# Performance work log

Measured on AMD Instinct MI355X. Metric: run time of the kernel, lower is better.

Reference implementation:

```python
import jax, jax.numpy as jnp
import numpy as np

B, S, H = 4, 2048, 1024

def setup_inputs() -> dict:
    key = jax.random.key(0)
    k = jax.random.split(key, 5)
    scale = 1.0 / np.sqrt(H)
    return {
        "hidden": jax.random.normal(k[0], (B, S, H), dtype=jnp.float32),
        "mask": jnp.zeros((B, 1, S, S), dtype=jnp.float32),
        "R": jax.random.normal(k[1], (S, S), dtype=jnp.float32),
        "G_w": jax.random.normal(k[2], (H, H), dtype=jnp.float32) * scale,
        "G_b": jnp.zeros((H,), dtype=jnp.float32),
        "F_w": jax.random.normal(k[3], (H, H), dtype=jnp.float32) * scale,
        "F_b": jnp.zeros((H,), dtype=jnp.float32),
    }

def reference(hidden, mask, R, G_w, G_b, F_w, F_b):
    # scores: [B, S, S] = learned random bias + additive attention mask
    scores = R + mask[:, 0]
    probs = jax.nn.softmax(scores, axis=-1)  # dropout is identity in eval mode
    values = jnp.einsum('bsh,oh->bso', hidden, G_w) + G_b  # G_linear
    out = jnp.einsum('bqk,bkh->bqh', probs, values)
    out = jnp.einsum('bsh,oh->bso', out, F_w) + F_b  # final_linear
    return out
```

## Files before the change

### kernel.cpp

```cpp
#include <hip/hip_runtime.h>
#include <hip/hip_bf16.h>

typedef __bf16 bf16x8 __attribute__((ext_vector_type(8)));
typedef __bf16 bf16x4 __attribute__((ext_vector_type(4)));
typedef float  f32x4  __attribute__((ext_vector_type(4)));
typedef float  f32x16 __attribute__((ext_vector_type(16)));

#define GPTR(p) ((__attribute__((address_space(1))) void*)(p))
#define LPTR(p) ((__attribute__((address_space(3))) void*)(p))

__global__ __launch_bounds__(256) void cvt_kernel(const float* __restrict__ x,
                                                  __bf16* __restrict__ y, long n) {
    long i = ((long)blockIdx.x * 256 + threadIdx.x) * 8;
    if (i >= n) return;
    float4 a = *reinterpret_cast<const float4*>(x + i);
    float4 c = *reinterpret_cast<const float4*>(x + i + 4);
    bf16x8 o;
    o[0] = (__bf16)a.x; o[1] = (__bf16)a.y; o[2] = (__bf16)a.z; o[3] = (__bf16)a.w;
    o[4] = (__bf16)c.x; o[5] = (__bf16)c.y; o[6] = (__bf16)c.z; o[7] = (__bf16)c.w;
    *reinterpret_cast<bf16x8*>(y + i) = o;
}

__global__ __launch_bounds__(256) void transpose_cvt_kernel(const float* __restrict__ x,
                                                            __bf16* __restrict__ y, int n) {
    __shared__ float tile[64][65];
    const int bx = blockIdx.x * 64;
    const int by = blockIdx.y * 64;
    const int t = threadIdx.x;
    const int tr = t >> 4;
    const int tc = (t & 15) * 4;
#pragma unroll
    for (int i = 0; i < 4; i++) {
        float4 v = *reinterpret_cast<const float4*>(&x[(size_t)(by + tr + i * 16) * n + bx + tc]);
        tile[tr + i * 16][tc + 0] = v.x;
        tile[tr + i * 16][tc + 1] = v.y;
        tile[tr + i * 16][tc + 2] = v.z;
        tile[tr + i * 16][tc + 3] = v.w;
    }
    __syncthreads();
    const int wr = t >> 2;
    const int wc = (t & 3) * 16;
    bf16x8 o0, o1;
#pragma unroll
    for (int j = 0; j < 8; j++) o0[j] = (__bf16)tile[wc + j][wr];
#pragma unroll
    for (int j = 0; j < 8; j++) o1[j] = (__bf16)tile[wc + 8 + j][wr];
    *reinterpret_cast<bf16x8*>(&y[(size_t)(bx + wr) * n + by + wc]) = o0;
    *reinterpret_cast<bf16x8*>(&y[(size_t)(bx + wr) * n + by + wc + 8]) = o1;
}

__global__ __launch_bounds__(256) void gemv_bias_kernel(const float* __restrict__ Fw,
                                                        const float* __restrict__ Gb,
                                                        const float* __restrict__ Fb,
                                                        float* __restrict__ b2, int H) {
    const int o = blockIdx.x;
    float s = 0.f;
    for (int h = threadIdx.x; h < H; h += 256) s += Fw[(size_t)o * H + h] * Gb[h];
#pragma unroll
    for (int off = 32; off > 0; off >>= 1) s += __shfl_xor(s, off);
    __shared__ float ss[4];
    if ((threadIdx.x & 63) == 0) ss[threadIdx.x >> 6] = s;
    __syncthreads();
    if (threadIdx.x == 0) b2[o] = ss[0] + ss[1] + ss[2] + ss[3] + Fb[o];
}

__global__ __launch_bounds__(256) void softmax_kernel(const float* __restrict__ R,
                                                      const float* __restrict__ mask,
                                                      __bf16* __restrict__ P, int S) {
    const int q = blockIdx.x, b = blockIdx.y;
    const int t = threadIdx.x;
    const int lane = t & 63, wave = t >> 6;
    const float* rrow = R + (size_t)q * S;
    const float* mrow = mask + ((size_t)b * S + q) * (size_t)S;
    __bf16* prow = P + ((size_t)b * S + q) * (size_t)S;

    float v[8];
#pragma unroll
    for (int i = 0; i < 2; i++) {
        float4 r4 = *reinterpret_cast<const float4*>(rrow + t * 8 + i * 4);
        float4 m4 = *reinterpret_cast<const float4*>(mrow + t * 8 + i * 4);
        v[i * 4 + 0] = r4.x + m4.x;
        v[i * 4 + 1] = r4.y + m4.y;
        v[i * 4 + 2] = r4.z + m4.z;
        v[i * 4 + 3] = r4.w + m4.w;
    }
    float mx = v[0];
#pragma unroll
    for (int i = 1; i < 8; i++) mx = fmaxf(mx, v[i]);
#pragma unroll
    for (int off = 32; off > 0; off >>= 1) mx = fmaxf(mx, __shfl_xor(mx, off));
    __shared__ float smax[4], ssum[4];
    if (lane == 0) smax[wave] = mx;
    __syncthreads();
    mx = fmaxf(fmaxf(smax[0], smax[1]), fmaxf(smax[2], smax[3]));
    float sum = 0.f;
#pragma unroll
    for (int i = 0; i < 8; i++) { v[i] = __expf(v[i] - mx); sum += v[i]; }
#pragma unroll
    for (int off = 32; off > 0; off >>= 1) sum += __shfl_xor(sum, off);
    if (lane == 0) ssum[wave] = sum;
    __syncthreads();
    sum = ssum[0] + ssum[1] + ssum[2] + ssum[3];
    const float inv = 1.0f / sum;
    bf16x8 o;
#pragma unroll
    for (int i = 0; i < 8; i++) o[i] = (__bf16)(v[i] * inv);
    *reinterpret_cast<bf16x8*>(prow + t * 8) = o;
}

template <bool TRANSC, bool CFLOAT, bool BIAS>
__global__ __launch_bounds__(256) void gemm_nt_kernel(
    const __bf16* __restrict__ A, const __bf16* __restrict__ B,
    const float* __restrict__ bias, void* __restrict__ Cv,
    int K, int lda, int ldb, int ldc,
    long strideA, long strideB, long strideC) {
    const int t = threadIdx.x;
    const int lane = t & 63;
    const int wave = t >> 6;
    const int lane31 = lane & 31;
    const int hi = lane >> 5;
    const int wm = (wave >> 1) * 64;
    const int wn = (wave & 1) * 64;
    const int bm = blockIdx.y * 128;
    const int bn = blockIdx.x * 128;
    const int bz = blockIdx.z;

    A += (size_t)bz * strideA;
    B += (size_t)bz * strideB;

    __shared__ __bf16 As[128 * 64];
    __shared__ __bf16 Bs[128 * 64];

    const int rsub = lane >> 3;
    const int csub = lane & 7;
    const int lchunk = csub ^ rsub;
    const __bf16* ga0 = A + (size_t)(bm + wave * 32 + rsub) * lda + lchunk * 8;
    const __bf16* gb0 = B + (size_t)(bn + wave * 32 + rsub) * ldb + lchunk * 8;

    f32x16 acc[2][2];
#pragma unroll
    for (int i = 0; i < 2; i++)
#pragma unroll
        for (int j = 0; j < 2; j++) acc[i][j] = (f32x16)(0.f);

    for (int kt = 0; kt < K; kt += 64) {
        __syncthreads();
#pragma unroll
        for (int c = 0; c < 4; c++)
            __builtin_amdgcn_global_load_lds(GPTR(ga0 + (size_t)(c * 8) * lda + kt),
                                             LPTR(&As[(wave * 32 + c * 8) * 64]), 16, 0, 0);
#pragma unroll
        for (int c = 0; c < 4; c++)
            __builtin_amdgcn_global_load_lds(GPTR(gb0 + (size_t)(c * 8) * ldb + kt),
                                             LPTR(&Bs[(wave * 32 + c * 8) * 64]), 16, 0, 0);
        __syncthreads();
#pragma unroll
        for (int s = 0; s < 4; s++) {
            bf16x8 af[2], bfr[2];
#pragma unroll
            for (int mi = 0; mi < 2; mi++) {
                const int r = wm + mi * 32 + lane31;
                af[mi] = *reinterpret_cast<const bf16x8*>(
                    &As[r * 64 + (((2 * s + hi) ^ (r & 7)) << 3)]);
            }
#pragma unroll
            for (int ni = 0; ni < 2; ni++) {
                const int r = wn + ni * 32 + lane31;
                bfr[ni] = *reinterpret_cast<const bf16x8*>(
                    &Bs[r * 64 + (((2 * s + hi) ^ (r & 7)) << 3)]);
            }
#pragma unroll
            for (int mi = 0; mi < 2; mi++)
#pragma unroll
                for (int ni = 0; ni < 2; ni++)
                    acc[mi][ni] = __builtin_amdgcn_mfma_f32_32x32x16_bf16(af[mi], bfr[ni], acc[mi][ni], 0, 0, 0);
        }
    }

    __bf16* Cb = (__bf16*)Cv + (size_t)bz * strideC;
    float* Cf = (float*)Cv + (size_t)bz * strideC;
#pragma unroll
    for (int mi = 0; mi < 2; mi++) {
#pragma unroll
        for (int ni = 0; ni < 2; ni++) {
            const int cm = bm + wm + mi * 32;
            const int cn = bn + wn + ni * 32 + lane31;
            const float bv = BIAS ? bias[cn] : 0.0f;
#pragma unroll
            for (int rq = 0; rq < 4; rq++) {
                const int rbase = rq * 8 + 4 * hi;
                if constexpr (TRANSC) {
                    bf16x4 pk;
#pragma unroll
                    for (int rr = 0; rr < 4; rr++) pk[rr] = (__bf16)(acc[mi][ni][rq * 4 + rr] + bv);
                    *reinterpret_cast<bf16x4*>(Cb + (size_t)cn * ldc + cm + rbase) = pk;
                } else if constexpr (CFLOAT) {
#pragma unroll
                    for (int rr = 0; rr < 4; rr++)
                        Cf[(size_t)(cm + rbase + rr) * ldc + cn] = acc[mi][ni][rq * 4 + rr] + bv;
                } else {
#pragma unroll
                    for (int rr = 0; rr < 4; rr++)
                        Cb[(size_t)(cm + rbase + rr) * ldc + cn] = (__bf16)(acc[mi][ni][rq * 4 + rr] + bv);
                }
            }
        }
    }
}

__global__ __launch_bounds__(256) void gemm_nt64_kernel(
    const __bf16* __restrict__ A, const __bf16* __restrict__ B,
    __bf16* __restrict__ C, int K, int lda, int ldb, int ldc) {
    const int t = threadIdx.x;
    const int lane = t & 63;
    const int wave = t >> 6;
    const int lane31 = lane & 31;
    const int hi = lane >> 5;
    const int wm = (wave >> 1) * 32;
    const int wn = (wave & 1) * 32;
    const int bm = blockIdx.y * 64;
    const int bn = blockIdx.x * 64;

    __shared__ __bf16 As[64 * 64];
    __shared__ __bf16 Bs[64 * 64];

    const int rsub = lane >> 3;
    const int csub = lane & 7;
    const int lchunk = csub ^ rsub;
    const __bf16* ga0 = A + (size_t)(bm + wave * 16 + rsub) * lda + lchunk * 8;
    const __bf16* gb0 = B + (size_t)(bn + wave * 16 + rsub) * ldb + lchunk * 8;

    f32x16 acc = (f32x16)(0.f);

    for (int kt = 0; kt < K; kt += 64) {
        __syncthreads();
#pragma unroll
        for (int c = 0; c < 2; c++)
            __builtin_amdgcn_global_load_lds(GPTR(ga0 + (size_t)(c * 8) * lda + kt),
                                             LPTR(&As[(wave * 16 + c * 8) * 64]), 16, 0, 0);
#pragma unroll
        for (int c = 0; c < 2; c++)
            __builtin_amdgcn_global_load_lds(GPTR(gb0 + (size_t)(c * 8) * ldb + kt),
                                             LPTR(&Bs[(wave * 16 + c * 8) * 64]), 16, 0, 0);
        __syncthreads();
#pragma unroll
        for (int s = 0; s < 4; s++) {
            const int ra = wm + lane31;
            const int rb = wn + lane31;
            bf16x8 af = *reinterpret_cast<const bf16x8*>(
                &As[ra * 64 + (((2 * s + hi) ^ (ra & 7)) << 3)]);
            bf16x8 bfr = *reinterpret_cast<const bf16x8*>(
                &Bs[rb * 64 + (((2 * s + hi) ^ (rb & 7)) << 3)]);
            acc = __builtin_amdgcn_mfma_f32_32x32x16_bf16(af, bfr, acc, 0, 0, 0);
        }
    }

    const int cm = bm + wm;
    const int cn = bn + wn + lane31;
#pragma unroll
    for (int rq = 0; rq < 4; rq++) {
        const int rbase = rq * 8 + 4 * hi;
#pragma unroll
        for (int rr = 0; rr < 4; rr++)
            C[(size_t)(cm + rbase + rr) * ldc + cn] = (__bf16)acc[rq * 4 + rr];
    }
}

extern "C" void kernel_launch(void* const* d_in, const int* in_sizes, int n_in,
                              void* d_out, int out_size, void* d_ws, size_t ws_size,
                              hipStream_t stream) {
    const float* hidden = (const float*)d_in[0];
    const float* mask   = (const float*)d_in[1];
    const float* R      = (const float*)d_in[2];
    const float* G_w    = (const float*)d_in[3];
    const float* G_b    = (const float*)d_in[4];
    const float* F_w    = (const float*)d_in[5];
    const float* F_b    = (const float*)d_in[6];
    float* out = (float*)d_out;

    constexpr int B = 4, S = 2048, H = 1024;
    char* ws = (char*)d_ws;
    __bf16* h_bf  = (__bf16*)(ws);
    __bf16* vt    = (__bf16*)(ws + (16ll << 20));
    __bf16* probs = (__bf16*)(ws + (32ll << 20));
    __bf16* Wm    = (__bf16*)(ws + (32ll << 20));
    __bf16* f_bf  = (__bf16*)(ws + (64ll << 20));
    __bf16* gt_bf = (__bf16*)(ws + (66ll << 20));
    float*  b2    = (float*)(ws + (64ll << 20));

    cvt_kernel<<<(H * H) / 8 / 256, 256, 0, stream>>>(F_w, f_bf, (long)H * H);
    transpose_cvt_kernel<<<dim3(H / 64, H / 64), 256, 0, stream>>>(G_w, gt_bf, H);

    gemm_nt64_kernel<<<dim3(H / 64, H / 64), 256, 0, stream>>>(
        f_bf, gt_bf, Wm, H, H, H, H);

    gemv_bias_kernel<<<H, 256, 0, stream>>>(F_w, G_b, F_b, b2, H);

    cvt_kernel<<<(B * S * H) / 8 / 256, 256, 0, stream>>>(hidden, h_bf, (long)B * S * H);

    gemm_nt_kernel<true, false, false><<<dim3(H / 128, S / 128, B), 256, 0, stream>>>(
        h_bf, Wm, nullptr, vt, H, H, H,  S,
        (long)S * H, 0, (long)H * S);

    softmax_kernel<<<dim3(S, B), 256, 0, stream>>>(R, mask, probs, S);

    gemm_nt_kernel<false, true, true><<<dim3(H / 128, S / 128, B), 256, 0, stream>>>(
        probs, vt, b2, out, S, S, S, H,
        (long)S * S, (long)H * S, (long)S * H);
}
```

Measured before the change: 257.1 us.

## Merge prep kernels into two phases, add XCD block swizzle and LDS-staged transposed store

Merges the conversion, transpose, bias GEMV, weight GEMM and softmax kernels into two multi-role launches. Blocks are dispatched by block index so independent work in each phase overlaps and fewer launches are needed. The final GEMM remaps its 1D block IDs so that blocks on the same XCD share a batch and row band, to improve L2 reuse. The transposed value GEMM now stages its output through LDS so that global writes are coalesced 16-byte stores instead of strided 8-byte ones. The cost is more divergent branching per launch and extra LDS traffic and barriers in the epilogue.

```diff
diff --git a/kernel.cpp b/kernel.cpp
--- a/kernel.cpp
+++ b/kernel.cpp
@@ -9,106 +9,171 @@
 #define GPTR(p) ((__attribute__((address_space(1))) void*)(p))
 #define LPTR(p) ((__attribute__((address_space(3))) void*)(p))
 
-__global__ __launch_bounds__(256) void cvt_kernel(const float* __restrict__ x,
-                                                  __bf16* __restrict__ y, long n) {
-    long i = ((long)blockIdx.x * 256 + threadIdx.x) * 8;
-    if (i >= n) return;
-    float4 a = *reinterpret_cast<const float4*>(x + i);
-    float4 c = *reinterpret_cast<const float4*>(x + i + 4);
-    bf16x8 o;
-    o[0] = (__bf16)a.x; o[1] = (__bf16)a.y; o[2] = (__bf16)a.z; o[3] = (__bf16)a.w;
-    o[4] = (__bf16)c.x; o[5] = (__bf16)c.y; o[6] = (__bf16)c.z; o[7] = (__bf16)c.w;
-    *reinterpret_cast<bf16x8*>(y + i) = o;
+__global__ __launch_bounds__(256) void phase_a_kernel(
+    const float* __restrict__ hidden, __bf16* __restrict__ h_bf,
+    const float* __restrict__ Fw, __bf16* __restrict__ f_bf,
+    const float* __restrict__ Gw, __bf16* __restrict__ gt_bf,
+    const float* __restrict__ Gb, const float* __restrict__ Fb,
+    float* __restrict__ b2, int H) {
+    __shared__ float tile[64][65];
+    const int blk = blockIdx.x;
+    const int t = threadIdx.x;
+
+    if (blk < 4096) {
+        long i = ((long)blk * 256 + t) * 8;
+        float4 a = *reinterpret_cast<const float4*>(hidden + i);
+        float4 c = *reinterpret_cast<const float4*>(hidden + i + 4);
+        bf16x8 o;
+        o[0] = (__bf16)a.x; o[1] = (__bf16)a.y; o[2] = (__bf16)a.z; o[3] = (__bf16)a.w;
+        o[4] = (__bf16)c.x; o[5] = (__bf16)c.y; o[6] = (__bf16)c.z; o[7] = (__bf16)c.w;
+        *reinterpret_cast<bf16x8*>(h_bf + i) = o;
+    } else if (blk < 4608) {
+        long i = ((long)(blk - 4096) * 256 + t) * 8;
+        float4 a = *reinterpret_cast<const float4*>(Fw + i);
+        float4 c = *reinterpret_cast<const float4*>(Fw + i + 4);
+        bf16x8 o;
+        o[0] = (__bf16)a.x; o[1] = (__bf16)a.y; o[2] = (__bf16)a.z; o[3] = (__bf16)a.w;
+        o[4] = (__bf16)c.x; o[5] = (__bf16)c.y; o[6] = (__bf16)c.z; o[7] = (__bf16)c.w;
+        *reinterpret_cast<bf16x8*>(f_bf + i) = o;
+    } else if (blk < 4864) {
+        const int id = blk - 4608;
+        const int bx = (id & 15) * 64;
+        const int by = (id >> 4) * 64;
+        const int tr = t >> 4;
+        const int tc = (t & 15) * 4;
+#pragma unroll
+        for (int i = 0; i < 4; i++) {
+            float4 v = *reinterpret_cast<const float4*>(&Gw[(size_t)(by + tr + i * 16) * H + bx + tc]);
+            tile[tr + i * 16][tc + 0] = v.x;
+            tile[tr + i * 16][tc + 1] = v.y;
+            tile[tr + i * 16][tc + 2] = v.z;
+            tile[tr + i * 16][tc + 3] = v.w;
+        }
+        __syncthreads();
+        const int wr = t >> 2;
+        const int wc = (t & 3) * 16;
+        bf16x8 o0, o1;
+#pragma unroll
+        for (int j = 0; j < 8; j++) o0[j] = (__bf16)tile[wc + j][wr];
+#pragma unroll
+        for (int j = 0; j < 8; j++) o1[j] = (__bf16)tile[wc + 8 + j][wr];
+        *reinterpret_cast<bf16x8*>(&gt_bf[(size_t)(bx + wr) * H + by + wc]) = o0;
+        *reinterpret_cast<bf16x8*>(&gt_bf[(size_t)(bx + wr) * H + by + wc + 8]) = o1;
+    } else {
+        const int o = blk - 4864;
+        float s = 0.f;
+        for (int h = t; h < H; h += 256) s += Fw[(size_t)o * H + h] * Gb[h];
+#pragma unroll
+        for (int off = 32; off > 0; off >>= 1) s += __shfl_xor(s, off);
+        __shared__ float ss[4];
+        if ((t & 63) == 0) ss[t >> 6] = s;
+        __syncthreads();
+        if (t == 0) b2[o] = ss[0] + ss[1] + ss[2] + ss[3] + Fb[o];
+    }
 }
 
-__global__ __launch_bounds__(256) void transpose_cvt_kernel(const float* __restrict__ x,
-                                                            __bf16* __restrict__ y, int n) {
-    __shared__ float tile[64][65];
-    const int bx = blockIdx.x * 64;
-    const int by = blockIdx.y * 64;
+__global__ __launch_bounds__(256) void phase_b_kernel(
+    const __bf16* __restrict__ f_bf, const __bf16* __restrict__ gt_bf,
+    __bf16* __restrict__ Wm, const float* __restrict__ R,
+    const float* __restrict__ mask, __bf16* __restrict__ P, int H, int S) {
+    const int blk = blockIdx.x;
     const int t = threadIdx.x;
-    const int tr = t >> 4;
-    const int tc = (t & 15) * 4;
-#pragma unroll
-    for (int i = 0; i < 4; i++) {
-        float4 v = *reinterpret_cast<const float4*>(&x[(size_t)(by + tr + i * 16) * n + bx + tc]);
-        tile[tr + i * 16][tc + 0] = v.x;
-        tile[tr + i * 16][tc + 1] = v.y;
-        tile[tr + i * 16][tc + 2] = v.z;
-        tile[tr + i * 16][tc + 3] = v.w;
-    }
-    __syncthreads();
-    const int wr = t >> 2;
-    const int wc = (t & 3) * 16;
-    bf16x8 o0, o1;
-#pragma unroll
-    for (int j = 0; j < 8; j++) o0[j] = (__bf16)tile[wc + j][wr];
-#pragma unroll
-    for (int j = 0; j < 8; j++) o1[j] = (__bf16)tile[wc + 8 + j][wr];
-    *reinterpret_cast<bf16x8*>(&y[(size_t)(bx + wr) * n + by + wc]) = o0;
-    *reinterpret_cast<bf16x8*>(&y[(size_t)(bx + wr) * n + by + wc + 8]) = o1;
+
+    if (blk < 256) {
+        __shared__ __bf16 As[64 * 64];
+        __shared__ __bf16 Bs[64 * 64];
+        const int lane = t & 63;
+        const int wave = t >> 6;
+        const int lane31 = lane & 31;
+        const int hi = lane >> 5;
+        const int wm = (wave >> 1) * 32;
+        const int wn = (wave & 1) * 32;
+        const int bm = (blk >> 4) * 64;
+        const int bn = (blk & 15) * 64;
+
+        const int rsub = lane >> 3;
+        const int csub = lane & 7;
+        const int lchunk = csub ^ rsub;
+        const __bf16* ga0 = f_bf + (size_t)(bm + wave * 16 + rsub) * H + lchunk * 8;
+        const __bf16* gb0 = gt_bf + (size_t)(bn + wave * 16 + rsub) * H + lchunk * 8;
+
+        f32x16 acc = (f32x16)(0.f);
+        for (int kt = 0; kt < H; kt += 64) {
+            __syncthreads();
+#pragma unroll
+            for (int c = 0; c < 2; c++)
+                __builtin_amdgcn_global_load_lds(GPTR(ga0 + (size_t)(c * 8) * H + kt),
+                                                 LPTR(&As[(wave * 16 + c * 8) * 64]), 16, 0, 0);
+#pragma unroll
+            for (int c = 0; c < 2; c++)
+                __builtin_amdgcn_global_load_lds(GPTR(gb0 + (size_t)(c * 8) * H + kt),
+                                                 LPTR(&Bs[(wave * 16 + c * 8) * 64]), 16, 0, 0);
+            __syncthreads();
+#pragma unroll
+            for (int s = 0; s < 4; s++) {
+                const int ra = wm + lane31;
+                const int rb = wn + lane31;
+                bf16x8 af = *reinterpret_cast<const bf16x8*>(
+                    &As[ra * 64 + (((2 * s + hi) ^ (ra & 7)) << 3)]);
+                bf16x8 bfr = *reinterpret_cast<const bf16x8*>(
+                    &Bs[rb * 64 + (((2 * s + hi) ^ (rb & 7)) << 3)]);
+                acc = __builtin_amdgcn_mfma_f32_32x32x16_bf16(af, bfr, acc, 0, 0, 0);
+            }
+        }
+        const int cm = bm + wm;
+        const int cn = bn + wn + lane31;
+#pragma unroll
+        for (int rq = 0; rq < 4; rq++) {
+            const int rbase = rq * 8 + 4 * hi;
+#pragma unroll
+            for (int rr = 0; rr < 4; rr++)
+                Wm[(size_t)(cm + rbase + rr) * H + cn] = (__bf16)acc[rq * 4 + rr];
+        }
+    } else {
+        const int id = blk - 256;
+        const int b = id >> 11;
+        const int q = id & 2047;
+        const int lane = t & 63, wave = t >> 6;
+        const float* rrow = R + (size_t)q * S;
+        const float* mrow = mask + ((size_t)b * S + q) * (size_t)S;
+        __bf16* prow = P + ((size_t)b * S + q) * (size_t)S;
+
+        float v[8];
+#pragma unroll
+        for (int i = 0; i < 2; i++) {
+            float4 r4 = *reinterpret_cast<const float4*>(rrow + t * 8 + i * 4);
+            float4 m4 = *reinterpret_cast<const float4*>(mrow + t * 8 + i * 4);
+            v[i * 4 + 0] = r4.x + m4.x;
+            v[i * 4 + 1] = r4.y + m4.y;
+            v[i * 4 + 2] = r4.z + m4.z;
+            v[i * 4 + 3] = r4.w + m4.w;
+        }
+        float mx = v[0];
+#pragma unroll
+        for (int i = 1; i < 8; i++) mx = fmaxf(mx, v[i]);
+#pragma unroll
+        for (int off = 32; off > 0; off >>= 1) mx = fmaxf(mx, __shfl_xor(mx, off));
+        __shared__ float smax[4], ssum[4];
+        if (lane == 0) smax[wave] = mx;
+        __syncthreads();
+        mx = fmaxf(fmaxf(smax[0], smax[1]), fmaxf(smax[2], smax[3]));
+        float sum = 0.f;
+#pragma unroll
+        for (int i = 0; i < 8; i++) { v[i] = __expf(v[i] - mx); sum += v[i]; }
+#pragma unroll
+        for (int off = 32; off > 0; off >>= 1) sum += __shfl_xor(sum, off);
+        if (lane == 0) ssum[wave] = sum;
+        __syncthreads();
+        sum = ssum[0] + ssum[1] + ssum[2] + ssum[3];
+        const float inv = 1.0f / sum;
+        bf16x8 o;
+#pragma unroll
+        for (int i = 0; i < 8; i++) o[i] = (__bf16)(v[i] * inv);
+        *reinterpret_cast<bf16x8*>(prow + t * 8) = o;
+    }
 }
 
-__global__ __launch_bounds__(256) void gemv_bias_kernel(const float* __restrict__ Fw,
-                                                        const float* __restrict__ Gb,
-                                                        const float* __restrict__ Fb,
-                                                        float* __restrict__ b2, int H) {
-    const int o = blockIdx.x;
-    float s = 0.f;
-    for (int h = threadIdx.x; h < H; h += 256) s += Fw[(size_t)o * H + h] * Gb[h];
-#pragma unroll
-    for (int off = 32; off > 0; off >>= 1) s += __shfl_xor(s, off);
-    __shared__ float ss[4];
-    if ((threadIdx.x & 63) == 0) ss[threadIdx.x >> 6] = s;
-    __syncthreads();
-    if (threadIdx.x == 0) b2[o] = ss[0] + ss[1] + ss[2] + ss[3] + Fb[o];
-}
-
-__global__ __launch_bounds__(256) void softmax_kernel(const float* __restrict__ R,
-                                                      const float* __restrict__ mask,
-                                                      __bf16* __restrict__ P, int S) {
-    const int q = blockIdx.x, b = blockIdx.y;
-    const int t = threadIdx.x;
-    const int lane = t & 63, wave = t >> 6;
-    const float* rrow = R + (size_t)q * S;
-    const float* mrow = mask + ((size_t)b * S + q) * (size_t)S;
-    __bf16* prow = P + ((size_t)b * S + q) * (size_t)S;
-
-    float v[8];
-#pragma unroll
-    for (int i = 0; i < 2; i++) {
-        float4 r4 = *reinterpret_cast<const float4*>(rrow + t * 8 + i * 4);
-        float4 m4 = *reinterpret_cast<const float4*>(mrow + t * 8 + i * 4);
-        v[i * 4 + 0] = r4.x + m4.x;
-        v[i * 4 + 1] = r4.y + m4.y;
-        v[i * 4 + 2] = r4.z + m4.z;
-        v[i * 4 + 3] = r4.w + m4.w;
-    }
-    float mx = v[0];
-#pragma unroll
-    for (int i = 1; i < 8; i++) mx = fmaxf(mx, v[i]);
-#pragma unroll
-    for (int off = 32; off > 0; off >>= 1) mx = fmaxf(mx, __shfl_xor(mx, off));
-    __shared__ float smax[4], ssum[4];
-    if (lane == 0) smax[wave] = mx;
-    __syncthreads();
-    mx = fmaxf(fmaxf(smax[0], smax[1]), fmaxf(smax[2], smax[3]));
-    float sum = 0.f;
-#pragma unroll
-    for (int i = 0; i < 8; i++) { v[i] = __expf(v[i] - mx); sum += v[i]; }
-#pragma unroll
-    for (int off = 32; off > 0; off >>= 1) sum += __shfl_xor(sum, off);
-    if (lane == 0) ssum[wave] = sum;
-    __syncthreads();
-    sum = ssum[0] + ssum[1] + ssum[2] + ssum[3];
-    const float inv = 1.0f / sum;
-    bf16x8 o;
-#pragma unroll
-    for (int i = 0; i < 8; i++) o[i] = (__bf16)(v[i] * inv);
-    *reinterpret_cast<bf16x8*>(prow + t * 8) = o;
-}
-
-template <bool TRANSC, bool CFLOAT, bool BIAS>
+template <bool TRANSC, bool CFLOAT, bool BIAS, bool SWZ>
 __global__ __launch_bounds__(256) void gemm_nt_kernel(
     const __bf16* __restrict__ A, const __bf16* __restrict__ B,
     const float* __restrict__ bias, void* __restrict__ Cv,
@@ -121,15 +186,26 @@
     const int hi = lane >> 5;
     const int wm = (wave >> 1) * 64;
     const int wn = (wave & 1) * 64;
-    const int bm = blockIdx.y * 128;
-    const int bn = blockIdx.x * 128;
-    const int bz = blockIdx.z;
+    int bm, bn, bz;
+    if constexpr (SWZ) {
+        const int id = blockIdx.x;
+        const int xcd = id & 7;
+        const int slot = id >> 3;
+        bz = xcd >> 1;
+        bm = ((xcd & 1) * 8 + (slot >> 3)) * 128;
+        bn = (slot & 7) * 128;
+    } else {
+        bm = blockIdx.y * 128;
+        bn = blockIdx.x * 128;
+        bz = blockIdx.z;
+    }
 
     A += (size_t)bz * strideA;
     B += (size_t)bz * strideB;
 
-    __shared__ __bf16 As[128 * 64];
-    __shared__ __bf16 Bs[128 * 64];
+    __shared__ __bf16 smem[TRANSC ? 16640 : 16384];
+    __bf16* As = smem;
+    __bf16* Bs = smem + 8192;
 
     const int rsub = lane >> 3;
     const int csub = lane & 7;
@@ -177,92 +253,55 @@
         }
     }
 
-    __bf16* Cb = (__bf16*)Cv + (size_t)bz * strideC;
-    float* Cf = (float*)Cv + (size_t)bz * strideC;
-#pragma unroll
-    for (int mi = 0; mi < 2; mi++) {
-#pragma unroll
-        for (int ni = 0; ni < 2; ni++) {
-            const int cm = bm + wm + mi * 32;
-            const int cn = bn + wn + ni * 32 + lane31;
-            const float bv = BIAS ? bias[cn] : 0.0f;
-#pragma unroll
-            for (int rq = 0; rq < 4; rq++) {
-                const int rbase = rq * 8 + 4 * hi;
-                if constexpr (TRANSC) {
+    if constexpr (TRANSC) {
+        __syncthreads();
+        __bf16* sC = smem;
+#pragma unroll
+        for (int mi = 0; mi < 2; mi++)
+#pragma unroll
+            for (int ni = 0; ni < 2; ni++)
+#pragma unroll
+                for (int rq = 0; rq < 4; rq++) {
+                    const int n_l = wn + ni * 32 + lane31;
+                    const int m_l = wm + mi * 32 + rq * 8 + 4 * hi;
                     bf16x4 pk;
 #pragma unroll
-                    for (int rr = 0; rr < 4; rr++) pk[rr] = (__bf16)(acc[mi][ni][rq * 4 + rr] + bv);
-                    *reinterpret_cast<bf16x4*>(Cb + (size_t)cn * ldc + cm + rbase) = pk;
-                } else if constexpr (CFLOAT) {
-#pragma unroll
-                    for (int rr = 0; rr < 4; rr++)
-                        Cf[(size_t)(cm + rbase + rr) * ldc + cn] = acc[mi][ni][rq * 4 + rr] + bv;
-                } else {
-#pragma unroll
-                    for (int rr = 0; rr < 4; rr++)
-                        Cb[(size_t)(cm + rbase + rr) * ldc + cn] = (__bf16)(acc[mi][ni][rq * 4 + rr] + bv);
+                    for (int rr = 0; rr < 4; rr++) pk[rr] = (__bf16)acc[mi][ni][rq * 4 + rr];
+                    *reinterpret_cast<bf16x4*>(&sC[n_l * 130 + m_l]) = pk;
+                }
+        __syncthreads();
+        __bf16* Ct = (__bf16*)Cv + (size_t)bz * strideC;
+        const int col = (t & 15) * 8;
+#pragma unroll
+        for (int p = 0; p < 8; p++) {
+            const int row = p * 16 + (t >> 4);
+            bf16x8 v = *reinterpret_cast<const bf16x8*>(&sC[row * 130 + col]);
+            *reinterpret_cast<bf16x8*>(Ct + (size_t)(bn + row) * ldc + bm + col) = v;
+        }
+    } else {
+        __bf16* Cb = (__bf16*)Cv + (size_t)bz * strideC;
+        float* Cf = (float*)Cv + (size_t)bz * strideC;
+#pragma unroll
+        for (int mi = 0; mi < 2; mi++)
+#pragma unroll
+            for (int ni = 0; ni < 2; ni++) {
+                const int cm = bm + wm + mi * 32;
+                const int cn = bn + wn + ni * 32 + lane31;
+                const float bv = BIAS ? bias[cn] : 0.0f;
+#pragma unroll
+                for (int rq = 0; rq < 4; rq++) {
+                    const int rbase = rq * 8 + 4 * hi;
+                    if constexpr (CFLOAT) {
+#pragma unroll
+                        for (int rr = 0; rr < 4; rr++)
+                            Cf[(size_t)(cm + rbase + rr) * ldc + cn] = acc[mi][ni][rq * 4 + rr] + bv;
+                    } else {
+#pragma unroll
+                        for (int rr = 0; rr < 4; rr++)
+                            Cb[(size_t)(cm + rbase + rr) * ldc + cn] = (__bf16)(acc[mi][ni][rq * 4 + rr] + bv);
+                    }
                 }
             }
-        }
-    }
-}
-
-__global__ __launch_bounds__(256) void gemm_nt64_kernel(
-    const __bf16* __restrict__ A, const __bf16* __restrict__ B,
-    __bf16* __restrict__ C, int K, int lda, int ldb, int ldc) {
-    const int t = threadIdx.x;
-    const int lane = t & 63;
-    const int wave = t >> 6;
-    const int lane31 = lane & 31;
-    const int hi = lane >> 5;
-    const int wm = (wave >> 1) * 32;
-    const int wn = (wave & 1) * 32;
-    const int bm = blockIdx.y * 64;
-    const int bn = blockIdx.x * 64;
-
-    __shared__ __bf16 As[64 * 64];
-    __shared__ __bf16 Bs[64 * 64];
-
-    const int rsub = lane >> 3;
-    const int csub = lane & 7;
-    const int lchunk = csub ^ rsub;
-    const __bf16* ga0 = A + (size_t)(bm + wave * 16 + rsub) * lda + lchunk * 8;
-    const __bf16* gb0 = B + (size_t)(bn + wave * 16 + rsub) * ldb + lchunk * 8;
-
-    f32x16 acc = (f32x16)(0.f);
-
-    for (int kt = 0; kt < K; kt += 64) {
-        __syncthreads();
-#pragma unroll
-        for (int c = 0; c < 2; c++)
-            __builtin_amdgcn_global_load_lds(GPTR(ga0 + (size_t)(c * 8) * lda + kt),
-                                             LPTR(&As[(wave * 16 + c * 8) * 64]), 16, 0, 0);
-#pragma unroll
-        for (int c = 0; c < 2; c++)
-            __builtin_amdgcn_global_load_lds(GPTR(gb0 + (size_t)(c * 8) * ldb + kt),
-                                             LPTR(&Bs[(wave * 16 + c * 8) * 64]), 16, 0, 0);
-        __syncthreads();
-#pragma unroll
-        for (int s = 0; s < 4; s++) {
-            const int ra = wm + lane31;
-            const int rb = wn + lane31;
-            bf16x8 af = *reinterpret_cast<const bf16x8*>(
-                &As[ra * 64 + (((2 * s + hi) ^ (ra & 7)) << 3)]);
-            bf16x8 bfr = *reinterpret_cast<const bf16x8*>(
-                &Bs[rb * 64 + (((2 * s + hi) ^ (rb & 7)) << 3)]);
-            acc = __builtin_amdgcn_mfma_f32_32x32x16_bf16(af, bfr, acc, 0, 0, 0);
-        }
-    }
-
-    const int cm = bm + wm;
-    const int cn = bn + wn + lane31;
-#pragma unroll
-    for (int rq = 0; rq < 4; rq++) {
-        const int rbase = rq * 8 + 4 * hi;
-#pragma unroll
-        for (int rr = 0; rr < 4; rr++)
-            C[(size_t)(cm + rbase + rr) * ldc + cn] = (__bf16)acc[rq * 4 + rr];
     }
 }
 
@@ -283,28 +322,21 @@
     __bf16* h_bf  = (__bf16*)(ws);
     __bf16* vt    = (__bf16*)(ws + (16ll << 20));
     __bf16* probs = (__bf16*)(ws + (32ll << 20));
-    __bf16* Wm    = (__bf16*)(ws + (32ll << 20));
     __bf16* f_bf  = (__bf16*)(ws + (64ll << 20));
     __bf16* gt_bf = (__bf16*)(ws + (66ll << 20));
-    float*  b2    = (float*)(ws + (64ll << 20));
-
-    cvt_kernel<<<(H * H) / 8 / 256, 256, 0, stream>>>(F_w, f_bf, (long)H * H);
-    transpose_cvt_kernel<<<dim3(H / 64, H / 64), 256, 0, stream>>>(G_w, gt_bf, H);
-
-    gemm_nt64_kernel<<<dim3(H / 64, H / 64), 256, 0, stream>>>(
-        f_bf, gt_bf, Wm, H, H, H, H);
-
-    gemv_bias_kernel<<<H, 256, 0, stream>>>(F_w, G_b, F_b, b2, H);
-
-    cvt_kernel<<<(B * S * H) / 8 / 256, 256, 0, stream>>>(hidden, h_bf, (long)B * S * H);
-
-    gemm_nt_kernel<true, false, false><<<dim3(H / 128, S / 128, B), 256, 0, stream>>>(
+    __bf16* Wm    = (__bf16*)(ws + (68ll << 20));
+    float*  b2    = (float*)(ws + (70ll << 20));
+
+    phase_a_kernel<<<5888, 256, 0, stream>>>(hidden, h_bf, F_w, f_bf, G_w, gt_bf,
+                                             G_b, F_b, b2, H);
+
+    phase_b_kernel<<<256 + B * S, 256, 0, stream>>>(f_bf, gt_bf, Wm, R, mask, probs, H, S);
+
+    gemm_nt_kernel<true, false, false, false><<<dim3(H / 128, S / 128, B), 256, 0, stream>>>(
         h_bf, Wm, nullptr, vt, H, H, H,  S,
         (long)S * H, 0, (long)H * S);
 
-    softmax_kernel<<<dim3(S, B), 256, 0, stream>>>(R, mask, probs, S);
-
-    gemm_nt_kernel<false, true, true><<<dim3(H / 128, S / 128, B), 256, 0, stream>>>(
+    gemm_nt_kernel<false, true, true, true><<<512, 256, 0, stream>>>(
         probs, vt, b2, out, S, S, S, H,
         (long)S * S, (long)H * S, (long)S * H);
 }
```

New measurement: 241.1 us. 1.07x faster.
